# Kernel tuning notes

Hardware: AMD Instinct MI355X
Metric: run time of the kernel (lower is better)

The kernel has to match this reference:

```python
import jax, jax.numpy as jnp
import numpy as np

B, L, C = 128, 256, 126   # batch, prior_len, code_dim
D = C + 2                 # encoder width = filt_dim (Time2Vector adds 2 channels)
H, DK, DV, FF = 8, 64, 64, 512
NL = 3                    # three stacked TransformerEncoder blocks


def setup_inputs() -> dict:
    key = jax.random.key(0)
    ks = iter(jax.random.split(key, 40))
    s = 0.05
    rn = lambda shape: jax.random.normal(next(ks), shape, jnp.float32) * s
    inp = {
        "x": jax.random.normal(next(ks), (B, L, C), jnp.float32),
        # Time2Vector params (per-timestep scalars)
        "wl": rn((L,)), "bl": rn((L,)), "wp": rn((L,)), "bp": rn((L,)),
        # per-encoder, per-head attention projections, stacked [NL, H, ...]
        "Wq": rn((NL, H, D, DK)), "bq": rn((NL, H, DK)),
        "Wk": rn((NL, H, D, DK)), "bk": rn((NL, H, DK)),
        "Wv": rn((NL, H, D, DV)), "bv": rn((NL, H, DV)),
        # output projection after head concat
        "Wo": rn((NL, H * DV, D)), "bo": rn((NL, D)),
        # LayerNorm 1
        "g1": jnp.ones((NL, D), jnp.float32), "be1": jnp.zeros((NL, D), jnp.float32),
        # Conv1D(kernel_size=1) FFN == dense
        "W1": rn((NL, D, FF)), "b1": rn((NL, FF)),
        "W2": rn((NL, FF, D)), "b2": rn((NL, D)),
        # LayerNorm 2
        "g2": jnp.ones((NL, D), jnp.float32), "be2": jnp.zeros((NL, D), jnp.float32),
        # head denses
        "dW1": rn((L * D, 512)), "db1": rn((512,)),
        "dW2": rn((512, C)), "db2": rn((C,)),
    }
    return inp


def _ln(x, g, b, eps=1e-6):
    m = jnp.mean(x, axis=-1, keepdims=True)
    v = jnp.var(x, axis=-1, keepdims=True)
    return g * (x - m) * jax.lax.rsqrt(v + eps) + b


def reference(x, wl, bl, wp, bp, Wq, bq, Wk, bk, Wv, bv, Wo, bo,
              g1, be1, W1, b1, W2, b2, g2, be2, dW1, db1, dW2, db2):
    # Time2Vector: mean over features, linear + periodic channels
    t = jnp.mean(x, axis=-1)                                   # [B, L]
    te = jnp.stack([wl * t + bl, jnp.sin(wp * t + bp)], axis=-1)  # [B, L, 2]
    h = jnp.concatenate([te, x], axis=-1)                      # [B, L, D]

    scale = 1.0 / np.sqrt(DK)
    for i in range(NL):
        q = jnp.einsum('bld,hdk->bhlk', h, Wq[i]) + bq[i][:, None, :]
        k = jnp.einsum('bld,hdk->bhlk', h, Wk[i]) + bk[i][:, None, :]
        v = jnp.einsum('bld,hdk->bhlk', h, Wv[i]) + bv[i][:, None, :]
        att = jax.nn.softmax(jnp.einsum('bhqk,bhmk->bhqm', q, k) * scale, axis=-1)
        o = jnp.einsum('bhqm,bhmv->bhqv', att, v)              # [B, H, L, DV]
        o = o.transpose(0, 2, 1, 3).reshape(B, L, H * DV)      # concat heads
        attn_out = o @ Wo[i] + bo[i]                           # [B, L, D]
        h1 = _ln(h + attn_out, g1[i], be1[i])
        ff = jax.nn.relu(h1 @ W1[i] + b1[i]) @ W2[i] + b2[i]
        # NOTE: original residual uses the ENCODER INPUT (inputs[0]), not h1
        h = _ln(h + ff, g2[i], be2[i])

    f = h.reshape(B, L * D)
    out = jax.nn.relu(f @ dW1 + db1) @ dW2 + db2               # [B, C]
    return out
```

## Files before the change

### kernel.cpp

```cpp
#include <hip/hip_runtime.h>
#include <hip/hip_bf16.h>

#define BB 128
#define LL 256
#define CC 126
#define DD 128
#define HH 8
#define FFF 512
#define NLL 3

typedef __bf16 bf16x8 __attribute__((ext_vector_type(8)));
typedef float  f32x4  __attribute__((ext_vector_type(4)));

static __device__ __forceinline__ f32x4 mfma16(bf16x8 a, bf16x8 b, f32x4 c) {
    return __builtin_amdgcn_mfma_f32_16x16x32_bf16(a, b, c, 0, 0, 0);
}

__global__ void pack_qkv(const float* __restrict__ Wq, const float* __restrict__ Wk,
                         const float* __restrict__ Wv, const float* __restrict__ bq,
                         const float* __restrict__ bk, const float* __restrict__ bv,
                         __bf16* __restrict__ Wt, float* __restrict__ bqk, float* __restrict__ bvp)
{
    int idx = blockIdx.x * 256 + threadIdx.x;
    if (idx >= NLL * 1536 * 128) return;
    int i = idx / (1536 * 128);
    int r = idx % (1536 * 128);
    int c = r >> 7, d = r & 127;
    int which = c >> 9, hh = (c >> 6) & 7, kk = c & 63;
    const float* W = (which == 0) ? Wq : (which == 1) ? Wk : Wv;
    Wt[idx] = (__bf16)W[(((size_t)i * HH + hh) * DD + d) * 64 + kk];
    if (d == 0) {
        float bvv = ((which == 0) ? bq : (which == 1) ? bk : bv)[(i * HH + hh) * 64 + kk];
        if (which < 2) bqk[i * 1024 + c] = bvv;
        else           bvp[i * 512 + (c - 1024)] = bvv;
    }
}

__global__ void pack_ffn(const float* __restrict__ Wo, const float* __restrict__ W1,
                         const float* __restrict__ W2, __bf16* __restrict__ Wot,
                         __bf16* __restrict__ W1t, __bf16* __restrict__ W2t)
{
    int idx = blockIdx.x * 256 + threadIdx.x;
    if (idx >= 3 * NLL * 65536) return;
    int which = idx / (NLL * 65536);
    int r = idx % (NLL * 65536);
    int i = r / 65536, e = r % 65536;
    if (which == 0) {
        int dout = e >> 9, hv = e & 511;
        Wot[(size_t)i * 65536 + e] = (__bf16)Wo[(size_t)i * 65536 + hv * 128 + dout];
    } else if (which == 1) {
        int f = e >> 7, d = e & 127;
        W1t[(size_t)i * 65536 + e] = (__bf16)W1[(size_t)i * 65536 + d * 512 + f];
    } else {
        int d = e >> 9, f = e & 511;
        W2t[(size_t)i * 65536 + e] = (__bf16)W2[(size_t)i * 65536 + f * 128 + d];
    }
}

__global__ __launch_bounds__(256) void trans_dw1(const float* __restrict__ src, __bf16* __restrict__ dst)
{
    __shared__ __bf16 tile[64][65];
    int bx = blockIdx.x;
    int by = blockIdx.y;
    int tc = threadIdx.x & 63, tr = threadIdx.x >> 6;
    #pragma unroll
    for (int i = 0; i < 16; i++) {
        int r = i * 4 + tr;
        tile[tc][r] = (__bf16)src[(size_t)(by * 64 + r) * 512 + bx * 64 + tc];
    }
    __syncthreads();
    #pragma unroll
    for (int i = 0; i < 16; i++) {
        int r = i * 4 + tr;
        dst[(size_t)(bx * 64 + r) * 32768 + by * 64 + tc] = tile[r][tc];
    }
}

__global__ __launch_bounds__(256) void t2v_k(const float* __restrict__ x,
                                             const float* __restrict__ wl, const float* __restrict__ bl,
                                             const float* __restrict__ wp, const float* __restrict__ bp,
                                             float* __restrict__ h, __bf16* __restrict__ hb)
{
    int w = threadIdx.x >> 6, lane = threadIdx.x & 63;
    int row = blockIdx.x * 4 + w;
    int l = row & (LL - 1);
    const float* xr = x + (size_t)row * CC;
    float sum = xr[lane];
    if (lane + 64 < CC) sum += xr[lane + 64];
    #pragma unroll
    for (int off = 32; off; off >>= 1) sum += __shfl_xor(sum, off);
    float t = sum * (1.0f / CC);
    float* hr = h + (size_t)row * DD;
    __bf16* hbr = hb + (size_t)row * DD;
    #pragma unroll
    for (int cc = 0; cc < 2; cc++) {
        int c = lane * 2 + cc;
        float v;
        if (c == 0)      v = wl[l] * t + bl[l];
        else if (c == 1) v = sinf(wp[l] * t + bp[l]);
        else             v = xr[c - 2];
        hr[c] = v;
        hbr[c] = (__bf16)v;
    }
}

template <typename TC, int BIASMODE, bool RELU, bool ATOMIC>
__global__ __launch_bounds__(256) void mgemm(const __bf16* __restrict__ A, const __bf16* __restrict__ Bt,
                                             const float* __restrict__ bias, TC* __restrict__ C,
                                             int M, int N, int K, int ldc, int KC)
{
    __shared__ __bf16 As[128][72];
    __shared__ __bf16 Bs[128][72];
    const int t = threadIdx.x;
    const int lane = t & 63, w = t >> 6;
    const int wr = w >> 1, wc = w & 1;
    const int col = lane & 15, g = lane >> 4;
    const int m0 = blockIdx.y * 128, n0 = blockIdx.x * 128;
    const int kbeg = blockIdx.z * KC;
    const int kend = min(K, kbeg + KC);
    f32x4 acc[4][4] = {};

    for (int kt = kbeg; kt < kend; kt += 64) {
        #pragma unroll
        for (int i = 0; i < 4; i++) {
            int c = i * 256 + t;
            int r = c >> 3, cc = c & 7;
            *reinterpret_cast<uint4*>(&As[r][cc * 8]) =
                *reinterpret_cast<const uint4*>(A + (size_t)(m0 + r) * K + kt + cc * 8);
            *reinterpret_cast<uint4*>(&Bs[r][cc * 8]) =
                *reinterpret_cast<const uint4*>(Bt + (size_t)(n0 + r) * K + kt + cc * 8);
        }
        __syncthreads();
        #pragma unroll
        for (int ks = 0; ks < 2; ks++) {
            bf16x8 af[4], bfr[4];
            #pragma unroll
            for (int mt = 0; mt < 4; mt++)
                af[mt] = *reinterpret_cast<const bf16x8*>(&As[wr * 64 + mt * 16 + col][ks * 32 + g * 8]);
            #pragma unroll
            for (int nt = 0; nt < 4; nt++)
                bfr[nt] = *reinterpret_cast<const bf16x8*>(&Bs[wc * 64 + nt * 16 + col][ks * 32 + g * 8]);
            #pragma unroll
            for (int mt = 0; mt < 4; mt++)
                #pragma unroll
                for (int nt = 0; nt < 4; nt++)
                    acc[mt][nt] = mfma16(af[mt], bfr[nt], acc[mt][nt]);
        }
        __syncthreads();
    }

    #pragma unroll
    for (int mt = 0; mt < 4; mt++) {
        #pragma unroll
        for (int nt = 0; nt < 4; nt++) {
            #pragma unroll
            for (int r = 0; r < 4; r++) {
                int m = m0 + wr * 64 + mt * 16 + g * 4 + r;
                int n = n0 + wc * 64 + nt * 16 + col;
                float v = acc[mt][nt][r];
                if constexpr (ATOMIC) {
                    atomicAdd((float*)&C[(size_t)m * ldc + n], v);
                } else {
                    if constexpr (BIASMODE == 1) v += bias[n];
                    if constexpr (BIASMODE == 2) v += bias[m];
                    if constexpr (RELU) v = fmaxf(v, 0.f);
                    if constexpr (__is_same(TC, float)) C[(size_t)m * ldc + n] = v;
                    else                                C[(size_t)m * ldc + n] = (__bf16)v;
                }
            }
        }
    }
}

__global__ __launch_bounds__(256, 2) void mattn(const __bf16* __restrict__ qkv,
                                                const __bf16* __restrict__ Vt,
                                                __bf16* __restrict__ obuf)
{
    __shared__ __bf16 Ks[256][72];
    __shared__ __bf16 Vs[64][264];
    __shared__ __bf16 P[4][16][72];
    const int t = threadIdx.x;
    const int lane = t & 63, w = t >> 6;
    const int col = lane & 15, g = lane >> 4;
    const int h = blockIdx.x & 7, b = blockIdx.x >> 3;
    const size_t tb = (size_t)b * 256;

    #pragma unroll
    for (int i = 0; i < 8; i++) {
        int e = i * 256 + t;
        int r = e >> 3, c = e & 7;
        *reinterpret_cast<uint4*>(&Ks[r][c * 8]) =
            *reinterpret_cast<const uint4*>(qkv + (tb + r) * 1024 + 512 + h * 64 + c * 8);
    }
    #pragma unroll
    for (int i = 0; i < 8; i++) {
        int e = i * 256 + t;
        int d = e >> 5, c = e & 31;
        *reinterpret_cast<uint4*>(&Vs[d][c * 8]) =
            *reinterpret_cast<const uint4*>(Vt + (size_t)(h * 64 + d) * 32768 + tb + c * 8);
    }
    __syncthreads();

    for (int qt = 0; qt < 4; qt++) {
        const int q0 = qt * 64 + w * 16;

        bf16x8 qf[2];
        #pragma unroll
        for (int ks = 0; ks < 2; ks++)
            qf[ks] = *reinterpret_cast<const bf16x8*>(
                qkv + (tb + q0 + col) * 1024 + h * 64 + ks * 32 + g * 8);

        f32x4 acc[16];
        #pragma unroll
        for (int nt = 0; nt < 16; nt++)
            acc[nt] = f32x4{0.f, 0.f, 0.f, 0.f};

        #pragma unroll
        for (int nt = 0; nt < 16; nt++) {
            bf16x8 kf0 = *reinterpret_cast<const bf16x8*>(&Ks[nt * 16 + col][g * 8]);
            bf16x8 kf1 = *reinterpret_cast<const bf16x8*>(&Ks[nt * 16 + col][32 + g * 8]);
            acc[nt] = mfma16(qf[0], kf0, acc[nt]);
            acc[nt] = mfma16(qf[1], kf1, acc[nt]);
        }

        float mx[4], den[4];
        #pragma unroll
        for (int r = 0; r < 4; r++) {
            float m = -1e30f;
            #pragma unroll
            for (int nt = 0; nt < 16; nt++) m = fmaxf(m, acc[nt][r]);
            #pragma unroll
            for (int off = 1; off < 16; off <<= 1) m = fmaxf(m, __shfl_xor(m, off));
            mx[r] = m;
        }
        #pragma unroll
        for (int r = 0; r < 4; r++) {
            float s = 0.f;
            #pragma unroll
            for (int nt = 0; nt < 16; nt++) {
                float p = __expf((acc[nt][r] - mx[r]) * 0.125f);
                acc[nt][r] = p;
                s += p;
            }
            #pragma unroll
            for (int off = 1; off < 16; off <<= 1) s += __shfl_xor(s, off);
            den[r] = s;
        }

        f32x4 o[4];
        #pragma unroll
        for (int dt = 0; dt < 4; dt++)
            o[dt] = f32x4{0.f, 0.f, 0.f, 0.f};

        #pragma unroll
        for (int kc = 0; kc < 4; kc++) {
            #pragma unroll
            for (int nt2 = 0; nt2 < 4; nt2++)
                #pragma unroll
                for (int r = 0; r < 4; r++)
                    P[w][g * 4 + r][nt2 * 16 + col] = (__bf16)acc[kc * 4 + nt2][r];

            #pragma unroll
            for (int ks = 0; ks < 2; ks++) {
                bf16x8 pf = *reinterpret_cast<const bf16x8*>(&P[w][col][ks * 32 + g * 8]);
                #pragma unroll
                for (int dt = 0; dt < 4; dt++) {
                    bf16x8 vf = *reinterpret_cast<const bf16x8*>(
                        &Vs[dt * 16 + col][kc * 64 + ks * 32 + g * 8]);
                    o[dt] = mfma16(pf, vf, o[dt]);
                }
            }
        }

        #pragma unroll
        for (int r = 0; r < 4; r++) {
            float inv = 1.f / den[r];
            #pragma unroll
            for (int dt = 0; dt < 4; dt++)
                obuf[(tb + q0 + g * 4 + r) * 512 + h * 64 + dt * 16 + col] =
                    (__bf16)(o[dt][r] * inv);
        }
    }
}

template <bool WF32>
__global__ __launch_bounds__(256) void ln_k(const float* __restrict__ X, const float* __restrict__ R,
                                            const float* __restrict__ g, const float* __restrict__ be,
                                            float* __restrict__ outf, __bf16* __restrict__ outb)
{
    int w = threadIdx.x >> 6, lane = threadIdx.x & 63;
    int row = blockIdx.x * 4 + w;
    const float* xr = X + (size_t)row * DD;
    const float* rr = R + (size_t)row * DD;
    float v0 = xr[lane] + rr[lane];
    float v1 = xr[lane + 64] + rr[lane + 64];
    float s = v0 + v1, sq = v0 * v0 + v1 * v1;
    #pragma unroll
    for (int off = 32; off; off >>= 1) { s += __shfl_xor(s, off); sq += __shfl_xor(sq, off); }
    float m = s * (1.f / DD);
    float var = sq * (1.f / DD) - m * m;
    float inv = rsqrtf(var + 1e-6f);
    float r0 = g[lane] * (v0 - m) * inv + be[lane];
    float r1 = g[lane + 64] * (v1 - m) * inv + be[lane + 64];
    if constexpr (WF32) {
        float* orow = outf + (size_t)row * DD;
        orow[lane] = r0; orow[lane + 64] = r1;
    }
    __bf16* brow = outb + (size_t)row * DD;
    brow[lane] = (__bf16)r0; brow[lane + 64] = (__bf16)r1;
}

__global__ void zero_k(float* p, int n)
{
    int i = blockIdx.x * 256 + threadIdx.x;
    if (i < n) p[i] = 0.f;
}

__global__ void biasrelu_k(float* p, const float* bias, int n, int ncols)
{
    int i = blockIdx.x * 256 + threadIdx.x;
    if (i < n) p[i] = fmaxf(p[i] + bias[i % ncols], 0.f);
}

__global__ __launch_bounds__(256) void gemm_f32(const float* __restrict__ A, const float* __restrict__ B,
                                                const float* __restrict__ bias, float* __restrict__ C,
                                                int M, int N, int K)
{
    __shared__ __align__(16) float As[16][64];
    __shared__ __align__(16) float Bs[16][64];
    const int t = threadIdx.x;
    const int tx = t & 15, ty = t >> 4;
    const int m0 = blockIdx.y * 64, n0 = blockIdx.x * 64;
    const int am = t >> 4, ak = t & 15;
    const int bk = t >> 6, bn = t & 63;
    float acc[4][4] = {};

    for (int kt = 0; kt < K; kt += 16) {
        #pragma unroll
        for (int i = 0; i < 4; i++)
            As[ak][i * 16 + am] = A[(size_t)(m0 + i * 16 + am) * K + kt + ak];
        #pragma unroll
        for (int i = 0; i < 4; i++) {
            int n = n0 + bn;
            Bs[i * 4 + bk][bn] = (n < N) ? B[(size_t)(kt + i * 4 + bk) * N + n] : 0.f;
        }
        __syncthreads();
        #pragma unroll
        for (int kk = 0; kk < 16; kk++) {
            float4 a4 = *reinterpret_cast<const float4*>(&As[kk][ty * 4]);
            float4 b4 = *reinterpret_cast<const float4*>(&Bs[kk][tx * 4]);
            float a[4] = {a4.x, a4.y, a4.z, a4.w};
            float b[4] = {b4.x, b4.y, b4.z, b4.w};
            #pragma unroll
            for (int i = 0; i < 4; i++)
                #pragma unroll
                for (int j = 0; j < 4; j++)
                    acc[i][j] = fmaf(a[i], b[j], acc[i][j]);
        }
        __syncthreads();
    }
    #pragma unroll
    for (int i = 0; i < 4; i++) {
        int m = m0 + ty * 4 + i;
        #pragma unroll
        for (int j = 0; j < 4; j++) {
            int n = n0 + tx * 4 + j;
            if (n < N && m < M) C[(size_t)m * N + n] = acc[i][j] + bias[n];
        }
    }
}

extern "C" void kernel_launch(void* const* d_in, const int* in_sizes, int n_in,
                              void* d_out, int out_size, void* d_ws, size_t ws_size,
                              hipStream_t stream)
{
    const float* x   = (const float*)d_in[0];
    const float* wl  = (const float*)d_in[1];
    const float* bl  = (const float*)d_in[2];
    const float* wp  = (const float*)d_in[3];
    const float* bp  = (const float*)d_in[4];
    const float* Wq  = (const float*)d_in[5];
    const float* bq  = (const float*)d_in[6];
    const float* Wk  = (const float*)d_in[7];
    const float* bk  = (const float*)d_in[8];
    const float* Wv  = (const float*)d_in[9];
    const float* bv  = (const float*)d_in[10];
    const float* Wo  = (const float*)d_in[11];
    const float* bo  = (const float*)d_in[12];
    const float* g1  = (const float*)d_in[13];
    const float* be1 = (const float*)d_in[14];
    const float* W1  = (const float*)d_in[15];
    const float* b1  = (const float*)d_in[16];
    const float* W2  = (const float*)d_in[17];
    const float* b2  = (const float*)d_in[18];
    const float* g2  = (const float*)d_in[19];
    const float* be2 = (const float*)d_in[20];
    const float* dW1 = (const float*)d_in[21];
    const float* db1 = (const float*)d_in[22];
    const float* dW2 = (const float*)d_in[23];
    const float* db2 = (const float*)d_in[24];
    float* out = (float*)d_out;

    char* ws = (char*)d_ws;
    float*  h_f32   = (float*)(ws);
    float*  tmp     = (float*)(ws + 16777216);
    __bf16* h_b     = (__bf16*)(ws + 33554432);
    __bf16* h1_b    = (__bf16*)(ws + 41943040);
    __bf16* qkv     = (__bf16*)(ws + 50331648);
    __bf16* buf512  = (__bf16*)(ws + 117440512);
    __bf16* obuf    = (__bf16*)(ws + 150994944);
    __bf16* Wtqkv   = (__bf16*)(ws + 184549376);
    __bf16* Wot     = (__bf16*)(ws + 185729024);
    __bf16* W1t     = (__bf16*)(ws + 186122240);
    __bf16* W2t     = (__bf16*)(ws + 186515456);
    float*  bqk     = (float*)(ws + 186908672);
    float*  bvp     = (float*)(ws + 186920960);
    float*  t1      = (float*)(ws + 186927104);
    __bf16* dW1t    = obuf;

    pack_qkv<<<(NLL * 1536 * 128 + 255) / 256, 256, 0, stream>>>(Wq, Wk, Wv, bq, bk, bv, Wtqkv, bqk, bvp);
    pack_ffn<<<(3 * NLL * 65536 + 255) / 256, 256, 0, stream>>>(Wo, W1, W2, Wot, W1t, W2t);
    t2v_k<<<8192, 256, 0, stream>>>(x, wl, bl, wp, bp, h_f32, h_b);

    for (int i = 0; i < NLL; i++) {
        mgemm<__bf16, 1, false, false><<<dim3(8, 256, 1), 256, 0, stream>>>(
            h_b, Wtqkv + (size_t)i * 1536 * 128, bqk + i * 1024, qkv, 32768, 1024, 128, 1024, 128);
        mgemm<__bf16, 2, false, false><<<dim3(256, 4, 1), 256, 0, stream>>>(
            Wtqkv + (size_t)i * 1536 * 128 + 1024 * 128, h_b, bvp + i * 512, buf512, 512, 32768, 128, 32768, 128);
        mattn<<<dim3(BB * HH), 256, 0, stream>>>(qkv, buf512, obuf);
        mgemm<float, 1, false, false><<<dim3(1, 256, 1), 256, 0, stream>>>(
            obuf, Wot + (size_t)i * 65536, bo + i * DD, tmp, 32768, 128, 512, 128, 512);
        ln_k<false><<<8192, 256, 0, stream>>>(tmp, h_f32, g1 + i * DD, be1 + i * DD, nullptr, h1_b);
        mgemm<__bf16, 1, true, false><<<dim3(4, 256, 1), 256, 0, stream>>>(
            h1_b, W1t + (size_t)i * 65536, b1 + i * FFF, buf512, 32768, 512, 128, 512, 128);
        mgemm<float, 1, false, false><<<dim3(1, 256, 1), 256, 0, stream>>>(
            buf512, W2t + (size_t)i * 65536, b2 + i * DD, tmp, 32768, 128, 512, 128, 512);
        ln_k<true><<<8192, 256, 0, stream>>>(tmp, h_f32, g2 + i * DD, be2 + i * DD, h_f32, h_b);
    }

    trans_dw1<<<dim3(8, 512, 1), 256, 0, stream>>>(dW1, dW1t);
    zero_k<<<256, 256, 0, stream>>>(t1, 128 * 512);
    mgemm<float, 0, false, true><<<dim3(4, 1, 64), 256, 0, stream>>>(
        h_b, dW1t, nullptr, t1, 128, 512, 32768, 512, 512);
    biasrelu_k<<<256, 256, 0, stream>>>(t1, db1, 128 * 512, 512);
    gemm_f32<<<dim3(2, 2, 1), 256, 0, stream>>>(t1, dW2, db2, out, 128, 126, 512);
}
```

Baseline: 736.9 us.

## Fuse residual LayerNorm into output-projection and FFN2 GEMM epilogues; fuse head tail

Adds an MFMA GEMM kernel whose 128-row block covers the full 128-wide output, computing bias plus residual add and LayerNorm in the epilogue via shuffle and shared-memory row reductions. This replaces the separate float tmp write and LN kernel pass twice per layer. The head's bias+ReLU and small fp32 GEMM are merged into one per-row kernel. Costs: fewer blocks (256) for the fused GEMM, and heavier epilogue register use.

```diff
diff --git a/kernel.cpp b/kernel.cpp
--- a/kernel.cpp
+++ b/kernel.cpp
@@ -172,6 +172,101 @@
     }
 }
 
+template <bool WF32>
+__global__ __launch_bounds__(256) void mgemm_ln(const __bf16* __restrict__ A, const __bf16* __restrict__ Bt,
+                                                const float* __restrict__ bias, const float* __restrict__ resid,
+                                                const float* __restrict__ g_, const float* __restrict__ be,
+                                                float* __restrict__ outf, __bf16* __restrict__ outb, int K)
+{
+    __shared__ __bf16 As[128][72];
+    __shared__ __bf16 Bs[128][72];
+    __shared__ float lnp[128][2][2];
+    const int t = threadIdx.x;
+    const int lane = t & 63, w = t >> 6;
+    const int wr = w >> 1, wc = w & 1;
+    const int col = lane & 15, g = lane >> 4;
+    const int m0 = blockIdx.x * 128;
+    f32x4 acc[4][4] = {};
+
+    for (int kt = 0; kt < K; kt += 64) {
+        #pragma unroll
+        for (int i = 0; i < 4; i++) {
+            int c = i * 256 + t;
+            int r = c >> 3, cc = c & 7;
+            *reinterpret_cast<uint4*>(&As[r][cc * 8]) =
+                *reinterpret_cast<const uint4*>(A + (size_t)(m0 + r) * K + kt + cc * 8);
+            *reinterpret_cast<uint4*>(&Bs[r][cc * 8]) =
+                *reinterpret_cast<const uint4*>(Bt + (size_t)r * K + kt + cc * 8);
+        }
+        __syncthreads();
+        #pragma unroll
+        for (int ks = 0; ks < 2; ks++) {
+            bf16x8 af[4], bfr[4];
+            #pragma unroll
+            for (int mt = 0; mt < 4; mt++)
+                af[mt] = *reinterpret_cast<const bf16x8*>(&As[wr * 64 + mt * 16 + col][ks * 32 + g * 8]);
+            #pragma unroll
+            for (int nt = 0; nt < 4; nt++)
+                bfr[nt] = *reinterpret_cast<const bf16x8*>(&Bs[wc * 64 + nt * 16 + col][ks * 32 + g * 8]);
+            #pragma unroll
+            for (int mt = 0; mt < 4; mt++)
+                #pragma unroll
+                for (int nt = 0; nt < 4; nt++)
+                    acc[mt][nt] = mfma16(af[mt], bfr[nt], acc[mt][nt]);
+        }
+        __syncthreads();
+    }
+
+    #pragma unroll
+    for (int mt = 0; mt < 4; mt++) {
+        #pragma unroll
+        for (int r = 0; r < 4; r++) {
+            int m = m0 + wr * 64 + mt * 16 + g * 4 + r;
+            float s = 0.f, q = 0.f;
+            #pragma unroll
+            for (int nt = 0; nt < 4; nt++) {
+                int n = wc * 64 + nt * 16 + col;
+                float v = acc[mt][nt][r] + bias[n] + resid[(size_t)m * DD + n];
+                acc[mt][nt][r] = v;
+                s += v;
+                q += v * v;
+            }
+            #pragma unroll
+            for (int off = 1; off < 16; off <<= 1) {
+                s += __shfl_xor(s, off);
+                q += __shfl_xor(q, off);
+            }
+            if (col == 0) {
+                int lm = wr * 64 + mt * 16 + g * 4 + r;
+                lnp[lm][wc][0] = s;
+                lnp[lm][wc][1] = q;
+            }
+        }
+    }
+    __syncthreads();
+
+    #pragma unroll
+    for (int mt = 0; mt < 4; mt++) {
+        #pragma unroll
+        for (int r = 0; r < 4; r++) {
+            int lm = wr * 64 + mt * 16 + g * 4 + r;
+            int m = m0 + lm;
+            float sum = lnp[lm][0][0] + lnp[lm][1][0];
+            float sq  = lnp[lm][0][1] + lnp[lm][1][1];
+            float mean = sum * (1.f / DD);
+            float var  = sq * (1.f / DD) - mean * mean;
+            float inv  = rsqrtf(var + 1e-6f);
+            #pragma unroll
+            for (int nt = 0; nt < 4; nt++) {
+                int n = wc * 64 + nt * 16 + col;
+                float rv = g_[n] * (acc[mt][nt][r] - mean) * inv + be[n];
+                if constexpr (WF32) outf[(size_t)m * DD + n] = rv;
+                outb[(size_t)m * DD + n] = (__bf16)rv;
+            }
+        }
+    }
+}
+
 __global__ __launch_bounds__(256, 2) void mattn(const __bf16* __restrict__ qkv,
                                                 const __bf16* __restrict__ Vt,
                                                 __bf16* __restrict__ obuf)
@@ -283,90 +378,30 @@
     }
 }
 
-template <bool WF32>
-__global__ __launch_bounds__(256) void ln_k(const float* __restrict__ X, const float* __restrict__ R,
-                                            const float* __restrict__ g, const float* __restrict__ be,
-                                            float* __restrict__ outf, __bf16* __restrict__ outb)
-{
-    int w = threadIdx.x >> 6, lane = threadIdx.x & 63;
-    int row = blockIdx.x * 4 + w;
-    const float* xr = X + (size_t)row * DD;
-    const float* rr = R + (size_t)row * DD;
-    float v0 = xr[lane] + rr[lane];
-    float v1 = xr[lane + 64] + rr[lane + 64];
-    float s = v0 + v1, sq = v0 * v0 + v1 * v1;
-    #pragma unroll
-    for (int off = 32; off; off >>= 1) { s += __shfl_xor(s, off); sq += __shfl_xor(sq, off); }
-    float m = s * (1.f / DD);
-    float var = sq * (1.f / DD) - m * m;
-    float inv = rsqrtf(var + 1e-6f);
-    float r0 = g[lane] * (v0 - m) * inv + be[lane];
-    float r1 = g[lane + 64] * (v1 - m) * inv + be[lane + 64];
-    if constexpr (WF32) {
-        float* orow = outf + (size_t)row * DD;
-        orow[lane] = r0; orow[lane + 64] = r1;
-    }
-    __bf16* brow = outb + (size_t)row * DD;
-    brow[lane] = (__bf16)r0; brow[lane + 64] = (__bf16)r1;
-}
-
 __global__ void zero_k(float* p, int n)
 {
     int i = blockIdx.x * 256 + threadIdx.x;
     if (i < n) p[i] = 0.f;
 }
 
-__global__ void biasrelu_k(float* p, const float* bias, int n, int ncols)
-{
-    int i = blockIdx.x * 256 + threadIdx.x;
-    if (i < n) p[i] = fmaxf(p[i] + bias[i % ncols], 0.f);
-}
-
-__global__ __launch_bounds__(256) void gemm_f32(const float* __restrict__ A, const float* __restrict__ B,
-                                                const float* __restrict__ bias, float* __restrict__ C,
-                                                int M, int N, int K)
-{
-    __shared__ __align__(16) float As[16][64];
-    __shared__ __align__(16) float Bs[16][64];
-    const int t = threadIdx.x;
-    const int tx = t & 15, ty = t >> 4;
-    const int m0 = blockIdx.y * 64, n0 = blockIdx.x * 64;
-    const int am = t >> 4, ak = t & 15;
-    const int bk = t >> 6, bn = t & 63;
-    float acc[4][4] = {};
-
-    for (int kt = 0; kt < K; kt += 16) {
-        #pragma unroll
-        for (int i = 0; i < 4; i++)
-            As[ak][i * 16 + am] = A[(size_t)(m0 + i * 16 + am) * K + kt + ak];
-        #pragma unroll
-        for (int i = 0; i < 4; i++) {
-            int n = n0 + bn;
-            Bs[i * 4 + bk][bn] = (n < N) ? B[(size_t)(kt + i * 4 + bk) * N + n] : 0.f;
-        }
-        __syncthreads();
-        #pragma unroll
-        for (int kk = 0; kk < 16; kk++) {
-            float4 a4 = *reinterpret_cast<const float4*>(&As[kk][ty * 4]);
-            float4 b4 = *reinterpret_cast<const float4*>(&Bs[kk][tx * 4]);
-            float a[4] = {a4.x, a4.y, a4.z, a4.w};
-            float b[4] = {b4.x, b4.y, b4.z, b4.w};
-            #pragma unroll
-            for (int i = 0; i < 4; i++)
-                #pragma unroll
-                for (int j = 0; j < 4; j++)
-                    acc[i][j] = fmaf(a[i], b[j], acc[i][j]);
-        }
-        __syncthreads();
-    }
-    #pragma unroll
-    for (int i = 0; i < 4; i++) {
-        int m = m0 + ty * 4 + i;
-        #pragma unroll
-        for (int j = 0; j < 4; j++) {
-            int n = n0 + tx * 4 + j;
-            if (n < N && m < M) C[(size_t)m * N + n] = acc[i][j] + bias[n];
-        }
+__global__ __launch_bounds__(256) void head2_k(const float* __restrict__ t1, const float* __restrict__ db1,
+                                               const float* __restrict__ dW2, const float* __restrict__ db2,
+                                               float* __restrict__ out)
+{
+    __shared__ float As[512];
+    const int m = blockIdx.x, t = threadIdx.x;
+    #pragma unroll
+    for (int i = 0; i < 2; i++) {
+        int k = i * 256 + t;
+        As[k] = fmaxf(t1[m * 512 + k] + db1[k], 0.f);
+    }
+    __syncthreads();
+    if (t < 126) {
+        float s = 0.f;
+        #pragma unroll 8
+        for (int k = 0; k < 512; k++)
+            s = fmaf(As[k], dW2[k * 126 + t], s);
+        out[m * 126 + t] = s + db2[t];
     }
 }
 
@@ -417,6 +452,7 @@
     float*  bvp     = (float*)(ws + 186920960);
     float*  t1      = (float*)(ws + 186927104);
     __bf16* dW1t    = obuf;
+    (void)tmp;
 
     pack_qkv<<<(NLL * 1536 * 128 + 255) / 256, 256, 0, stream>>>(Wq, Wk, Wv, bq, bk, bv, Wtqkv, bqk, bvp);
     pack_ffn<<<(3 * NLL * 65536 + 255) / 256, 256, 0, stream>>>(Wo, W1, W2, Wot, W1t, W2t);
@@ -428,20 +464,19 @@
         mgemm<__bf16, 2, false, false><<<dim3(256, 4, 1), 256, 0, stream>>>(
             Wtqkv + (size_t)i * 1536 * 128 + 1024 * 128, h_b, bvp + i * 512, buf512, 512, 32768, 128, 32768, 128);
         mattn<<<dim3(BB * HH), 256, 0, stream>>>(qkv, buf512, obuf);
-        mgemm<float, 1, false, false><<<dim3(1, 256, 1), 256, 0, stream>>>(
-            obuf, Wot + (size_t)i * 65536, bo + i * DD, tmp, 32768, 128, 512, 128, 512);
-        ln_k<false><<<8192, 256, 0, stream>>>(tmp, h_f32, g1 + i * DD, be1 + i * DD, nullptr, h1_b);
+        mgemm_ln<false><<<dim3(256), 256, 0, stream>>>(
+            obuf, Wot + (size_t)i * 65536, bo + i * DD, h_f32,
+            g1 + i * DD, be1 + i * DD, nullptr, h1_b, 512);
         mgemm<__bf16, 1, true, false><<<dim3(4, 256, 1), 256, 0, stream>>>(
             h1_b, W1t + (size_t)i * 65536, b1 + i * FFF, buf512, 32768, 512, 128, 512, 128);
-        mgemm<float, 1, false, false><<<dim3(1, 256, 1), 256, 0, stream>>>(
-            buf512, W2t + (size_t)i * 65536, b2 + i * DD, tmp, 32768, 128, 512, 128, 512);
-        ln_k<true><<<8192, 256, 0, stream>>>(tmp, h_f32, g2 + i * DD, be2 + i * DD, h_f32, h_b);
+        mgemm_ln<true><<<dim3(256), 256, 0, stream>>>(
+            buf512, W2t + (size_t)i * 65536, b2 + i * DD, h_f32,
+            g2 + i * DD, be2 + i * DD, h_f32, h_b, 512);
     }
 
     trans_dw1<<<dim3(8, 512, 1), 256, 0, stream>>>(dW1, dW1t);
     zero_k<<<256, 256, 0, stream>>>(t1, 128 * 512);
     mgemm<float, 0, false, true><<<dim3(4, 1, 64), 256, 0, stream>>>(
         h_b, dW1t, nullptr, t1, 128, 512, 32768, 512, 512);
-    biasrelu_k<<<256, 256, 0, stream>>>(t1, db1, 128 * 512, 512);
-    gemm_f32<<<dim3(2, 2, 1), 256, 0, stream>>>(t1, dW2, db2, out, 128, 126, 512);
-}
+    head2_k<<<dim3(128), 256, 0, stream>>>(t1, db1, dW2, db2, out);
+}
```

Result: faster. 695.9 us (-5.6%).
